# Kernel tuning notes

Hardware: AMD Instinct MI355X
Metric: run time of the kernel (lower is better)

## Reference

```python
import jax, jax.numpy as jnp
import numpy as np

N_NODES = 50000
N_EDGES = 800000
D = 128  # node_feat_size == edge_hidden_size


def setup_inputs() -> dict:
    key = jax.random.key(0)
    ks = jax.random.split(key, 10)
    return {
        "edge_logits": jax.random.normal(ks[0], (N_EDGES, 1), jnp.float32),
        "node_feats": jax.random.normal(ks[1], (N_NODES, D), jnp.float32),
        "src": jax.random.randint(ks[2], (N_EDGES,), 0, N_NODES),
        "dst": jax.random.randint(ks[3], (N_EDGES,), 0, N_NODES),
        "W_proj": jax.random.normal(ks[4], (D, D), jnp.float32) * 0.05,
        "b_proj": jax.random.normal(ks[5], (D,), jnp.float32) * 0.05,
        "W_ih": jax.random.normal(ks[6], (3 * D, D), jnp.float32) * 0.05,
        "b_ih": jax.random.normal(ks[7], (3 * D,), jnp.float32) * 0.05,
        "W_hh": jax.random.normal(ks[8], (3 * D, D), jnp.float32) * 0.05,
        "b_hh": jax.random.normal(ks[9], (3 * D,), jnp.float32) * 0.05,
    }


def reference(edge_logits, node_feats, src, dst, W_proj, b_proj, W_ih, b_ih, W_hh, b_hh):
    N = node_feats.shape[0]
    # --- edge softmax: normalize logits over incoming edges of each dst node ---
    emax = jax.ops.segment_max(edge_logits, dst, num_segments=N)      # [N,1]
    ex = jnp.exp(edge_logits - emax[dst])                             # [E,1]
    esum = jax.ops.segment_sum(ex, dst, num_segments=N)               # [N,1]
    a = ex / esum[dst]                                                # [E,1]
    # --- project nodes (dropout=0 -> identity), gather-multiply-scatter ---
    hv = node_feats @ W_proj.T + b_proj                               # [N,D]
    msg = hv[src] * a                                                 # [E,D]
    c = jax.ops.segment_sum(msg, dst, num_segments=N)                 # [N,D]
    context = jax.nn.elu(c)
    # --- GRUCell(input=context, hidden=node_feats), torch semantics ---
    gi = context @ W_ih.T + b_ih                                      # [N,3D]
    gh = node_feats @ W_hh.T + b_hh                                   # [N,3D]
    i_r, i_z, i_n = jnp.split(gi, 3, axis=-1)
    h_r, h_z, h_n = jnp.split(gh, 3, axis=-1)
    r = jax.nn.sigmoid(i_r + h_r)
    z = jax.nn.sigmoid(i_z + h_z)
    n = jnp.tanh(i_n + r * h_n)
    h_new = (1.0 - z) * n + z * node_feats
    return jax.nn.relu(h_new)
```

## Files before the change

kernel.cpp:

```cpp
#include <hip/hip_runtime.h>
#include <hip/hip_fp16.h>
#include <math.h>

#define NN 50000
#define NE 800000
#define DD 128
#define SLOT 64
#define FILLB 782
#define WPREP 578
#define NFCONV 6250

typedef short bf16x8 __attribute__((ext_vector_type(8)));
typedef float f32x4 __attribute__((ext_vector_type(4)));

#define GLOAD_LDS16(gp, lp) \
    __builtin_amdgcn_global_load_lds((const __attribute__((address_space(1))) void*)(gp), \
                                     (__attribute__((address_space(3))) void*)(lp), 16, 0, 0)

__device__ __forceinline__ unsigned short f2bf(float x) {
    unsigned u = __float_as_uint(x);
    unsigned r = (u + 0x7FFFu + ((u >> 16) & 1u)) >> 16;
    return (unsigned short)r;
}
__device__ __forceinline__ float bf2f(unsigned short b) {
    return __uint_as_float(((unsigned)b) << 16);
}
__device__ __forceinline__ unsigned pack2(float x, float y) {
    return (unsigned)f2bf(x) | ((unsigned)f2bf(y) << 16);
}
__device__ __forceinline__ unsigned short f2h(float x) {
    _Float16 h = (_Float16)x;
    return *reinterpret_cast<unsigned short*>(&h);
}
__device__ __forceinline__ float h2f(unsigned short u) {
    _Float16 h = *reinterpret_cast<_Float16*>(&u);
    return (float)h;
}

__device__ __forceinline__ float wbig_val(const float* Wih, const float* Whh, int r, int c) {
    if (r < 256)  return (c < 128) ? Wih[r * 128 + c] : Whh[r * 128 + (c - 128)];
    if (r < 384)  return (c < 128) ? Wih[r * 128 + c] : 0.f;
    return (c < 128) ? 0.f : Whh[(r - 128) * 128 + (c - 128)];
}

__global__ __launch_bounds__(256) void k_prepfill(const float* __restrict__ logits,
                                                  const int* __restrict__ src,
                                                  const int* __restrict__ dst,
                                                  int* __restrict__ cnt,
                                                  unsigned* __restrict__ csr,
                                                  const float* __restrict__ Wp,
                                                  const float* __restrict__ Wih,
                                                  const float* __restrict__ bih,
                                                  const float* __restrict__ Whh,
                                                  const float* __restrict__ bhh,
                                                  const float* __restrict__ nf,
                                                  unsigned short* __restrict__ Wfrag,
                                                  unsigned short* __restrict__ Wpfrag,
                                                  float* __restrict__ bbig,
                                                  unsigned* __restrict__ nfb) {
    if (blockIdx.x < FILLB) {
        int i4 = (blockIdx.x * 256 + threadIdx.x) * 4;
        if (i4 + 3 < NE) {
            float4 lg = *(const float4*)(logits + i4);
            int4 s = *(const int4*)(src + i4);
            int4 d = *(const int4*)(dst + i4);
            unsigned v0 = (unsigned)(unsigned short)s.x | ((unsigned)f2h(expf(lg.x)) << 16);
            unsigned v1 = (unsigned)(unsigned short)s.y | ((unsigned)f2h(expf(lg.y)) << 16);
            unsigned v2 = (unsigned)(unsigned short)s.z | ((unsigned)f2h(expf(lg.z)) << 16);
            unsigned v3 = (unsigned)(unsigned short)s.w | ((unsigned)f2h(expf(lg.w)) << 16);
            int p0 = atomicAdd(&cnt[d.x], 1);
            int p1 = atomicAdd(&cnt[d.y], 1);
            int p2 = atomicAdd(&cnt[d.z], 1);
            int p3 = atomicAdd(&cnt[d.w], 1);
            if (p0 < SLOT) csr[(size_t)d.x * SLOT + p0] = v0;
            if (p1 < SLOT) csr[(size_t)d.y * SLOT + p1] = v1;
            if (p2 < SLOT) csr[(size_t)d.z * SLOT + p2] = v2;
            if (p3 < SLOT) csr[(size_t)d.w * SLOT + p3] = v3;
        } else {
            for (int k = 0; k < 4 && i4 + k < NE; k++) {
                int e = i4 + k;
                unsigned v = (unsigned)(unsigned short)src[e] |
                             ((unsigned)f2h(expf(logits[e])) << 16);
                int pos = atomicAdd(&cnt[dst[e]], 1);
                if (pos < SLOT) csr[(size_t)dst[e] * SLOT + pos] = v;
            }
        }
    } else if (blockIdx.x < FILLB + WPREP) {
        int idx = (blockIdx.x - FILLB) * 256 + threadIdx.x;
        if (idx < 512 * 256) {
            int e = idx & 7, lane = (idx >> 3) & 63, ct = (idx >> 9) & 31, ks = idx >> 14;
            int r = ct * 16 + (lane & 15);
            int k = ks * 32 + (lane >> 4) * 8 + e;
            Wfrag[idx] = f2bf(wbig_val(Wih, Whh, r, k));
        } else if (idx < 512 * 256 + 128 * 128) {
            int i = idx - 512 * 256;
            int e = i & 7, lane = (i >> 3) & 63, ct = (i >> 9) & 7, ks = i >> 12;
            int r = ct * 16 + (lane & 15);
            int k = ks * 32 + (lane >> 4) * 8 + e;
            Wpfrag[i] = f2bf(Wp[r * 128 + k]);
        } else if (idx < 512 * 256 + 128 * 128 + 512) {
            int j = idx - (512 * 256 + 128 * 128);
            float v;
            if (j < 256)      v = bih[j] + bhh[j];
            else if (j < 384) v = bih[j];
            else              v = bhh[j - 128];
            bbig[j] = v;
        }
    } else {
        int t = (blockIdx.x - FILLB - WPREP) * 256 + threadIdx.x;
        float4 v = ((const float4*)nf)[t];
        nfb[t * 2 + 0] = pack2(v.x, v.y);
        nfb[t * 2 + 1] = pack2(v.z, v.w);
    }
}

__global__ __launch_bounds__(256, 2) void k_proj(const unsigned short* __restrict__ nfb,
                                                 const unsigned short* __restrict__ Wpfrag,
                                                 const float* __restrict__ bp,
                                                 unsigned short* __restrict__ hvb) {
    __shared__ unsigned short Bs[2][8 * 64 * 8];
    const int t = threadIdx.x;
    const int w = t >> 6;
    const int lane = t & 63;
    const int row0 = blockIdx.x * 64 + w * 16;
    const int rowA = min(row0 + (lane & 15), NN - 1);
    const int koff = (lane >> 4) * 8;

    bf16x8 a[4];
#pragma unroll
    for (int ks = 0; ks < 4; ks++)
        a[ks] = *reinterpret_cast<const bf16x8*>(nfb + (size_t)rowA * DD + ks * 32 + koff);

    f32x4 acc[8];
#pragma unroll
    for (int i = 0; i < 8; i++) acc[i] = (f32x4){0.f, 0.f, 0.f, 0.f};

#pragma unroll
    for (int i = 0; i < 2; i++)
        GLOAD_LDS16(Wpfrag + (size_t)(i * 256 + t) * 8, &Bs[0][(i * 256 + t) * 8]);
    __syncthreads();

#pragma unroll
    for (int ks = 0; ks < 4; ks++) {
        const int cur = ks & 1;
        if (ks < 3) {
#pragma unroll
            for (int i = 0; i < 2; i++)
                GLOAD_LDS16(Wpfrag + (size_t)(ks + 1) * 4096 + (i * 256 + t) * 8,
                            &Bs[cur ^ 1][(i * 256 + t) * 8]);
        }
#pragma unroll
        for (int ct = 0; ct < 8; ct++) {
            bf16x8 b = *reinterpret_cast<const bf16x8*>(&Bs[cur][(ct * 64 + lane) * 8]);
            acc[ct] = __builtin_amdgcn_mfma_f32_16x16x32_bf16(a[ks], b, acc[ct], 0, 0, 0);
        }
        __syncthreads();
    }
#pragma unroll
    for (int ct = 0; ct < 8; ct++) {
        int j = ct * 16 + (lane & 15);
        float bj = bp[j];
#pragma unroll
        for (int reg = 0; reg < 4; reg++) {
            int row = row0 + (lane >> 4) * 4 + reg;
            if (row < NN) hvb[(size_t)row * DD + j] = f2bf(acc[ct][reg] + bj);
        }
    }
}

__global__ __launch_bounds__(256) void k_aggr(const int* __restrict__ cnt,
                                              const unsigned* __restrict__ csr,
                                              const unsigned* __restrict__ hvb,
                                              unsigned* __restrict__ ctx_out) {
    const int n = blockIdx.x * 4 + (threadIdx.x >> 6);
    const int l = threadIdx.x & 63;
    const int beg = n * SLOT;
    const int deg = min(cnt[n], SLOT);
    const int end = beg + deg;
    float ax = 0.f, ay = 0.f, es = 0.f;
    int e = beg;
    for (; e + 8 <= end; e += 8) {
        unsigned c0 = csr[e + 0], c1 = csr[e + 1], c2 = csr[e + 2], c3 = csr[e + 3];
        unsigned c4 = csr[e + 4], c5 = csr[e + 5], c6 = csr[e + 6], c7 = csr[e + 7];
        unsigned h0 = hvb[(size_t)(c0 & 0xFFFF) * 64 + l];
        unsigned h1 = hvb[(size_t)(c1 & 0xFFFF) * 64 + l];
        unsigned h2 = hvb[(size_t)(c2 & 0xFFFF) * 64 + l];
        unsigned h3 = hvb[(size_t)(c3 & 0xFFFF) * 64 + l];
        unsigned h4 = hvb[(size_t)(c4 & 0xFFFF) * 64 + l];
        unsigned h5 = hvb[(size_t)(c5 & 0xFFFF) * 64 + l];
        unsigned h6 = hvb[(size_t)(c6 & 0xFFFF) * 64 + l];
        unsigned h7 = hvb[(size_t)(c7 & 0xFFFF) * 64 + l];
        float a0 = h2f((unsigned short)(c0 >> 16)), a1 = h2f((unsigned short)(c1 >> 16));
        float a2 = h2f((unsigned short)(c2 >> 16)), a3 = h2f((unsigned short)(c3 >> 16));
        float a4 = h2f((unsigned short)(c4 >> 16)), a5 = h2f((unsigned short)(c5 >> 16));
        float a6 = h2f((unsigned short)(c6 >> 16)), a7 = h2f((unsigned short)(c7 >> 16));
        es += ((a0 + a1) + (a2 + a3)) + ((a4 + a5) + (a6 + a7));
        ax += a0 * bf2f((unsigned short)(h0 & 0xFFFF));
        ay += a0 * bf2f((unsigned short)(h0 >> 16));
        ax += a1 * bf2f((unsigned short)(h1 & 0xFFFF));
        ay += a1 * bf2f((unsigned short)(h1 >> 16));
        ax += a2 * bf2f((unsigned short)(h2 & 0xFFFF));
        ay += a2 * bf2f((unsigned short)(h2 >> 16));
        ax += a3 * bf2f((unsigned short)(h3 & 0xFFFF));
        ay += a3 * bf2f((unsigned short)(h3 >> 16));
        ax += a4 * bf2f((unsigned short)(h4 & 0xFFFF));
        ay += a4 * bf2f((unsigned short)(h4 >> 16));
        ax += a5 * bf2f((unsigned short)(h5 & 0xFFFF));
        ay += a5 * bf2f((unsigned short)(h5 >> 16));
        ax += a6 * bf2f((unsigned short)(h6 & 0xFFFF));
        ay += a6 * bf2f((unsigned short)(h6 >> 16));
        ax += a7 * bf2f((unsigned short)(h7 & 0xFFFF));
        ay += a7 * bf2f((unsigned short)(h7 >> 16));
    }
    for (; e < end; e++) {
        unsigned c = csr[e];
        float a = h2f((unsigned short)(c >> 16));
        unsigned hv2 = hvb[(size_t)(c & 0xFFFF) * 64 + l];
        es += a;
        ax += a * bf2f((unsigned short)(hv2 & 0xFFFF));
        ay += a * bf2f((unsigned short)(hv2 >> 16));
    }
    float vx = 0.f, vy = 0.f;
    if (deg > 0) {
        float inv = 1.f / es;
        vx = ax * inv; vy = ay * inv;
        vx = vx > 0.f ? vx : expm1f(vx);
        vy = vy > 0.f ? vy : expm1f(vy);
    }
    ctx_out[(size_t)n * 128 + l] = pack2(vx, vy);
}

__global__ __launch_bounds__(256, 2) void k_gru(const unsigned short* __restrict__ nfb,
                                                const unsigned short* __restrict__ Wfrag,
                                                const float* __restrict__ bbig,
                                                float* __restrict__ out) {
    __shared__ unsigned short Bs[2][32 * 64 * 8];
    const int t = threadIdx.x;
    const int w = t >> 6;
    const int lane = t & 63;
    const int row0 = blockIdx.x * 64 + w * 16;
    const int rowA = min(row0 + (lane & 15), NN - 1);
    const int koff = (lane >> 4) * 8;
    const unsigned short* ctxo = (const unsigned short*)out;

    bf16x8 a[8];
#pragma unroll
    for (int ks = 0; ks < 4; ks++)
        a[ks] = *reinterpret_cast<const bf16x8*>(ctxo + (size_t)rowA * 256 + ks * 32 + koff);
#pragma unroll
    for (int ks = 0; ks < 4; ks++)
        a[4 + ks] = *reinterpret_cast<const bf16x8*>(nfb + (size_t)rowA * DD + ks * 32 + koff);

    f32x4 acc[32];
#pragma unroll
    for (int i = 0; i < 32; i++) acc[i] = (f32x4){0.f, 0.f, 0.f, 0.f};

#pragma unroll
    for (int i = 0; i < 8; i++)
        GLOAD_LDS16(Wfrag + (size_t)(i * 256 + t) * 8, &Bs[0][(i * 256 + t) * 8]);
    __syncthreads();

#pragma unroll
    for (int ks = 0; ks < 8; ks++) {
        const int cur = ks & 1;
        if (ks < 7) {
#pragma unroll
            for (int i = 0; i < 8; i++)
                GLOAD_LDS16(Wfrag + (size_t)(ks + 1) * 16384 + (i * 256 + t) * 8,
                            &Bs[cur ^ 1][(i * 256 + t) * 8]);
        }
#pragma unroll
        for (int ct = 0; ct < 32; ct++) {
            bf16x8 b = *reinterpret_cast<const bf16x8*>(&Bs[cur][(ct * 64 + lane) * 8]);
            acc[ct] = __builtin_amdgcn_mfma_f32_16x16x32_bf16(a[ks], b, acc[ct], 0, 0, 0);
        }
        __syncthreads();
    }

#pragma unroll
    for (int ct = 0; ct < 8; ct++) {
        int j = ct * 16 + (lane & 15);
        float bR = bbig[j];
        float bZ = bbig[128 + j];
        float bI = bbig[256 + j];
        float bH = bbig[384 + j];
#pragma unroll
        for (int reg = 0; reg < 4; reg++) {
            int row = row0 + (lane >> 4) * 4 + reg;
            if (row < NN) {
                float r = 1.f / (1.f + expf(-(acc[ct][reg] + bR)));
                float z = 1.f / (1.f + expf(-(acc[ct + 8][reg] + bZ)));
                float nn = tanhf(acc[ct + 16][reg] + bI + r * (acc[ct + 24][reg] + bH));
                float hp = bf2f(nfb[(size_t)row * DD + j]);
                float h = (1.f - z) * nn + z * hp;
                out[(size_t)row * DD + j] = fmaxf(h, 0.f);
            }
        }
    }
}

extern "C" void kernel_launch(void* const* d_in, const int* in_sizes, int n_in,
                              void* d_out, int out_size, void* d_ws, size_t ws_size,
                              hipStream_t stream) {
    const float* edge_logits = (const float*)d_in[0];
    const float* node_feats  = (const float*)d_in[1];
    const int*   src         = (const int*)d_in[2];
    const int*   dst         = (const int*)d_in[3];
    const float* Wp          = (const float*)d_in[4];
    const float* bp          = (const float*)d_in[5];
    const float* Wih         = (const float*)d_in[6];
    const float* bih         = (const float*)d_in[7];
    const float* Whh         = (const float*)d_in[8];
    const float* bhh         = (const float*)d_in[9];
    float* out = (float*)d_out;

    char* ws = (char*)d_ws;
    int*            cnt     = (int*)(ws);
    float*          bbig    = (float*)(ws + 512 * 1024);
    unsigned short* Wpfrag  = (unsigned short*)(ws + 1024 * 1024);
    unsigned short* Wfrag   = (unsigned short*)(ws + 1024 * 1024 + 64 * 1024);
    unsigned*       csr     = (unsigned*)(ws + 2 * 1024 * 1024);
    unsigned short* hvb     = (unsigned short*)(ws + 15 * 1024 * 1024);
    unsigned short* nfb     = (unsigned short*)(ws + 28 * 1024 * 1024);

    hipMemsetAsync(cnt, 0, NN * sizeof(int), stream);

    k_prepfill<<<FILLB + WPREP + NFCONV, 256, 0, stream>>>(
        edge_logits, src, dst, cnt, csr,
        Wp, Wih, bih, Whh, bhh, node_feats,
        Wfrag, Wpfrag, bbig, (unsigned*)nfb);
    k_proj<<<(NN + 63) / 64, 256, 0, stream>>>((const unsigned short*)nfb, Wpfrag, bp, hvb);
    k_aggr<<<NN / 4, 256, 0, stream>>>(cnt, csr, (const unsigned*)hvb, (unsigned*)out);
    k_gru<<<(NN + 63) / 64, 256, 0, stream>>>((const unsigned short*)nfb, Wfrag, bbig, out);
}
```

Baseline: 158.9 us.

## Partition CSR fill by destination range per XCD to localize atomics

Restructures the edge-to-CSR fill so each block handles a chunk of edges but only processes edges whose destination falls in one of eight node ranges, keyed by blockIdx & 7 to line up with the 8 XCDs. The aim is to keep the atomic counters and CSR slot writes for a destination range in a single XCD's L2, cutting cross-die traffic and atomic contention. The cost is that every block reads the dst array for its chunk, so dst is read eight times overall, and the block count doubles.

```diff
diff --git a/kernel.cpp b/kernel.cpp
--- a/kernel.cpp
+++ b/kernel.cpp
@@ -6,7 +6,9 @@
 #define NE 800000
 #define DD 128
 #define SLOT 64
-#define FILLB 782
+#define NXCD 8
+#define DRANGE 6250
+#define FILLB 1568
 #define WPREP 578
 #define NFCONV 6250
 
@@ -41,6 +43,17 @@
     if (r < 256)  return (c < 128) ? Wih[r * 128 + c] : Whh[r * 128 + (c - 128)];
     if (r < 384)  return (c < 128) ? Wih[r * 128 + c] : 0.f;
     return (c < 128) ? 0.f : Whh[(r - 128) * 128 + (c - 128)];
+}
+
+__device__ __forceinline__ void fill_one(const float* __restrict__ logits,
+                                         const int* __restrict__ src,
+                                         int* __restrict__ cnt,
+                                         unsigned* __restrict__ csr,
+                                         int e, int d) {
+    unsigned v = (unsigned)(unsigned short)src[e] |
+                 ((unsigned)f2h(expf(logits[e])) << 16);
+    int p = atomicAdd(&cnt[d], 1);
+    if (p < SLOT) csr[(size_t)d * SLOT + p] = v;
 }
 
 __global__ __launch_bounds__(256) void k_prepfill(const float* __restrict__ logits,
@@ -59,30 +72,27 @@
                                                   float* __restrict__ bbig,
                                                   unsigned* __restrict__ nfb) {
     if (blockIdx.x < FILLB) {
-        int i4 = (blockIdx.x * 256 + threadIdx.x) * 4;
-        if (i4 + 3 < NE) {
-            float4 lg = *(const float4*)(logits + i4);
-            int4 s = *(const int4*)(src + i4);
-            int4 d = *(const int4*)(dst + i4);
-            unsigned v0 = (unsigned)(unsigned short)s.x | ((unsigned)f2h(expf(lg.x)) << 16);
-            unsigned v1 = (unsigned)(unsigned short)s.y | ((unsigned)f2h(expf(lg.y)) << 16);
-            unsigned v2 = (unsigned)(unsigned short)s.z | ((unsigned)f2h(expf(lg.z)) << 16);
-            unsigned v3 = (unsigned)(unsigned short)s.w | ((unsigned)f2h(expf(lg.w)) << 16);
-            int p0 = atomicAdd(&cnt[d.x], 1);
-            int p1 = atomicAdd(&cnt[d.y], 1);
-            int p2 = atomicAdd(&cnt[d.z], 1);
-            int p3 = atomicAdd(&cnt[d.w], 1);
-            if (p0 < SLOT) csr[(size_t)d.x * SLOT + p0] = v0;
-            if (p1 < SLOT) csr[(size_t)d.y * SLOT + p1] = v1;
-            if (p2 < SLOT) csr[(size_t)d.z * SLOT + p2] = v2;
-            if (p3 < SLOT) csr[(size_t)d.w * SLOT + p3] = v3;
-        } else {
-            for (int k = 0; k < 4 && i4 + k < NE; k++) {
-                int e = i4 + k;
-                unsigned v = (unsigned)(unsigned short)src[e] |
-                             ((unsigned)f2h(expf(logits[e])) << 16);
-                int pos = atomicAdd(&cnt[dst[e]], 1);
-                if (pos < SLOT) csr[(size_t)dst[e] * SLOT + pos] = v;
+        const int g = blockIdx.x & 7;
+        const int chunk = blockIdx.x >> 3;
+        const int dlo = g * DRANGE;
+        const int dhi = min(dlo + DRANGE, NN);
+#pragma unroll
+        for (int i = 0; i < 4; i++) {
+            int e4 = chunk * 4096 + i * 1024 + (int)threadIdx.x * 4;
+            if (e4 + 3 < NE) {
+                int4 d = *(const int4*)(dst + e4);
+                if (d.x >= dlo && d.x < dhi) fill_one(logits, src, cnt, csr, e4 + 0, d.x);
+                if (d.y >= dlo && d.y < dhi) fill_one(logits, src, cnt, csr, e4 + 1, d.y);
+                if (d.z >= dlo && d.z < dhi) fill_one(logits, src, cnt, csr, e4 + 2, d.z);
+                if (d.w >= dlo && d.w < dhi) fill_one(logits, src, cnt, csr, e4 + 3, d.w);
+            } else {
+                for (int k = 0; k < 4; k++) {
+                    int e = e4 + k;
+                    if (e < NE) {
+                        int dd = dst[e];
+                        if (dd >= dlo && dd < dhi) fill_one(logits, src, cnt, csr, e, dd);
+                    }
+                }
             }
         }
     } else if (blockIdx.x < FILLB + WPREP) {
```

After: 147.2 us. 1.08x faster.
